# Kernel tuning notes

Measured on AMD Instinct MI355X. Metric: run time of the kernel, lower is better.

The kernel has to match this reference:

```python
import jax, jax.numpy as jnp
import numpy as np
from jax.ops import segment_sum, segment_max

N, E = 50000, 500000
D_IN, D_H, D_OUT = 128, 256, 40
BN_EPS = 1e-5


def setup_inputs() -> dict:
    key = jax.random.key(0)
    ks = jax.random.split(key, 16)
    g = lambda k, shape, fan: jax.random.normal(k, shape, jnp.float32) * (1.0 / np.sqrt(fan))
    inp = {
        "x": jax.random.normal(ks[0], (N, D_IN), jnp.float32),
        "edge_index": jax.random.randint(ks[1], (2, E), 0, N, jnp.int64),
        # GAT (heads=1)
        "W_gat": g(ks[2], (D_IN, D_H), D_IN),
        "att_src": g(ks[3], (D_H,), D_H),
        "att_dst": g(ks[4], (D_H,), D_H),
        "b_gat": jnp.zeros((D_H,), jnp.float32),
        # GIN MLP
        "W_gin1": g(ks[5], (D_IN, D_H), D_IN),
        "b_gin1": jnp.zeros((D_H,), jnp.float32),
        "W_gin2": g(ks[6], (D_H, D_H), D_H),
        "b_gin2": jnp.zeros((D_H,), jnp.float32),
        # GCN
        "W_gcn": g(ks[7], (D_IN, D_H), D_IN),
        "b_gcn": jnp.zeros((D_H,), jnp.float32),
        # BatchNorm1d(3*hidden)
        "gamma": jnp.ones((3 * D_H,), jnp.float32),
        "beta": jnp.zeros((3 * D_H,), jnp.float32),
        # head
        "W_lin": g(ks[8], (3 * D_H, D_H), 3 * D_H),
        "b_lin": jnp.zeros((D_H,), jnp.float32),
        "W_lin2": g(ks[9], (D_H, D_OUT), D_H),
        "b_lin2": jnp.zeros((D_OUT,), jnp.float32),
    }
    return inp


def _forward(x, edge_index, W_gat, att_src, att_dst, b_gat, W_gin1, b_gin1,
             W_gin2, b_gin2, W_gcn, b_gcn, gamma, beta, W_lin, b_lin, W_lin2, b_lin2):
    n = x.shape[0]
    src, dst = edge_index[0], edge_index[1]
    loop = jnp.arange(n, dtype=src.dtype)
    src_sl = jnp.concatenate([src, loop])  # edges + self-loops (GAT/GCN)
    dst_sl = jnp.concatenate([dst, loop])

    # ---- GATConv (1 head), messages src -> dst, softmax over dst ----
    xs = x @ W_gat                                   # [N, H]
    a = jax.nn.leaky_relu(xs @ att_src, negative_slope=0.2) if False else None
    e = (xs @ att_src)[src_sl] + (xs @ att_dst)[dst_sl]   # [E+N]
    e = jax.nn.leaky_relu(e, negative_slope=0.2)
    m = segment_max(e, dst_sl, num_segments=n)
    w = jnp.exp(e - m[dst_sl])
    denom = segment_sum(w, dst_sl, num_segments=n)
    alpha = w / denom[dst_sl]
    x_gat = segment_sum(alpha[:, None] * xs[src_sl], dst_sl, num_segments=n) + b_gat

    # ---- GINConv (eps=0): MLP(x + sum_neighbors x_j) ----
    agg = segment_sum(x[src], dst, num_segments=n)
    h = x + agg
    x_gin = jax.nn.relu(h @ W_gin1 + b_gin1) @ W_gin2 + b_gin2

    # ---- GCNConv: symmetric normalization with self-loops ----
    deg = segment_sum(jnp.ones_like(dst_sl, dtype=x.dtype), dst_sl, num_segments=n)
    dis = jax.lax.rsqrt(jnp.maximum(deg, 1.0))  # deg >= 1 due to self-loops
    norm = dis[src_sl] * dis[dst_sl]
    xw = x @ W_gcn
    x_gcn = segment_sum(norm[:, None] * xw[src_sl], dst_sl, num_segments=n) + b_gcn

    # ---- concat -> BN (training-mode batch stats) -> ReLU -> MLP head ----
    xc = jnp.concatenate([x_gat, x_gin, x_gcn], axis=1)  # [N, 3H]
    mu = jnp.mean(xc, axis=0)
    var = jnp.mean((xc - mu) ** 2, axis=0)
    xb = (xc - mu) * jax.lax.rsqrt(var + BN_EPS) * gamma + beta
    h2 = jax.nn.relu(jax.nn.relu(xb) @ W_lin + b_lin)
    return h2 @ W_lin2 + b_lin2


def reference(x, edge_index, W_gat, att_src, att_dst, b_gat, W_gin1, b_gin1,
              W_gin2, b_gin2, W_gcn, b_gcn, gamma, beta, W_lin, b_lin, W_lin2, b_lin2):
    return _forward(x, edge_index, W_gat, att_src, att_dst, b_gat, W_gin1, b_gin1,
                    W_gin2, b_gin2, W_gcn, b_gcn, gamma, beta, W_lin, b_lin, W_lin2, b_lin2)
```

## Files before the change

### kernel.cpp

```cpp
#include <hip/hip_runtime.h>
#include <math.h>

#define NN 50000
#define NE 500000

typedef __attribute__((ext_vector_type(8))) short short8;
typedef __attribute__((ext_vector_type(4))) float f32x4;

__device__ __forceinline__ float leaky02(float x) { return x > 0.f ? x : 0.2f * x; }
__device__ __forceinline__ ushort f2b(float f) {
    uint u = __float_as_uint(f);
    u += 0x7fffu + ((u >> 16) & 1u);
    return (ushort)(u >> 16);
}
__device__ __forceinline__ float b2f(ushort h) { return __uint_as_float(((uint)h) << 16); }
__device__ __forceinline__ float b2f_lo(uint w) { return __uint_as_float(w << 16); }
__device__ __forceinline__ float b2f_hi(uint w) { return __uint_as_float(w & 0xffff0000u); }
__device__ __forceinline__ uint pack2(float a, float b) {
    return (uint)f2b(a) | ((uint)f2b(b) << 16);
}

__global__ void mm_wt(const float* __restrict__ W, ushort* __restrict__ Wt, int K, int Nc)
{
    int idx = blockIdx.x * 256 + threadIdx.x;
    if (idx >= K * Nc) return;
    int n = idx / K, k = idx - n * K;
    Wt[idx] = f2b(W[(size_t)k * Nc + n]);
}

__global__ void mm_attvec(const float* __restrict__ W, const float* __restrict__ as_,
                          const float* __restrict__ ad_, float* __restrict__ va, float* __restrict__ vd)
{
    int i = threadIdx.x;
    const float* vec = (i < 128) ? as_ : ad_;
    int k = i & 127;
    float s = 0.f;
    for (int j = 0; j < 256; ++j) s += W[(size_t)k * 256 + j] * vec[j];
    if (i < 128) va[k] = s; else vd[k] = s;
}

__global__ __launch_bounds__(256) void mm_cvt_es(const float* __restrict__ x,
                                                 const float* __restrict__ va, const float* __restrict__ vd,
                                                 ushort* __restrict__ xb,
                                                 float* __restrict__ es, float* __restrict__ ed)
{
    int node = blockIdx.x * 4 + (threadIdx.x >> 6);
    int lane = threadIdx.x & 63;
    if (node >= NN) return;
    float2 xv = *(const float2*)(x + (size_t)node * 128 + lane * 2);
    float2 a = *(const float2*)(va + lane * 2);
    float2 b = *(const float2*)(vd + lane * 2);
    *(uint*)(xb + (size_t)node * 128 + lane * 2) = pack2(xv.x, xv.y);
    float s = xv.x * a.x + xv.y * a.y;
    float d = xv.x * b.x + xv.y * b.y;
    #pragma unroll
    for (int off = 32; off; off >>= 1) {
        s += __shfl_down(s, off);
        d += __shfl_down(d, off);
    }
    if (lane == 0) { es[node] = s; ed[node] = d; }
}

__global__ void mm_count(const int* __restrict__ dst, int* __restrict__ deg)
{
    int e = blockIdx.x * 256 + threadIdx.x;
    if (e >= NE) return;
    atomicAdd(&deg[dst[e]], 1);
}

__global__ __launch_bounds__(256) void mm_scan1(const int* __restrict__ deg, int* __restrict__ part)
{
    __shared__ int red[256];
    int i = blockIdx.x * 256 + threadIdx.x;
    red[threadIdx.x] = (i < NN) ? deg[i] : 0;
    __syncthreads();
    for (int off = 128; off; off >>= 1) {
        if (threadIdx.x < off) red[threadIdx.x] += red[threadIdx.x + off];
        __syncthreads();
    }
    if (threadIdx.x == 0) part[blockIdx.x] = red[0];
}

__global__ __launch_bounds__(256) void mm_scan2(int* __restrict__ part, int nb)
{
    __shared__ int tile[256];
    int t = threadIdx.x;
    int v = (t < nb) ? part[t] : 0;
    tile[t] = v; __syncthreads();
    for (int off = 1; off < 256; off <<= 1) {
        int a = (t >= off) ? tile[t - off] : 0;
        __syncthreads();
        tile[t] += a;
        __syncthreads();
    }
    if (t < nb) part[t] = tile[t] - v;
}

__global__ __launch_bounds__(256) void mm_scan3(const int* __restrict__ deg, const int* __restrict__ part,
                                                int* __restrict__ row_ptr, int* __restrict__ cursor)
{
    __shared__ int tile[256];
    int t = threadIdx.x;
    int i = blockIdx.x * 256 + t;
    int v = (i < NN) ? deg[i] : 0;
    tile[t] = v; __syncthreads();
    for (int off = 1; off < 256; off <<= 1) {
        int a = (t >= off) ? tile[t - off] : 0;
        __syncthreads();
        tile[t] += a;
        __syncthreads();
    }
    if (i < NN) {
        int ex = part[blockIdx.x] + tile[t] - v;
        row_ptr[i] = ex;
        cursor[i] = ex;
    }
    if (i == 0) row_ptr[NN] = NE;
}

__global__ void mm_fill(const int* __restrict__ src, const int* __restrict__ dst,
                        int* __restrict__ cursor, int* __restrict__ csr_src)
{
    int e = blockIdx.x * 256 + threadIdx.x;
    if (e >= NE) return;
    int pos = atomicAdd(&cursor[dst[e]], 1);
    csr_src[pos] = src[e];
}

__global__ void mm_dis(const int* __restrict__ row_ptr, float* __restrict__ dis)
{
    int i = blockIdx.x * 256 + threadIdx.x;
    if (i >= NN) return;
    dis[i] = rsqrtf((float)(row_ptr[i + 1] - row_ptr[i] + 1));
}

__global__ __launch_bounds__(256) void mm_node_agg(
    const int* __restrict__ row_ptr, const int* __restrict__ csr_src,
    const float* __restrict__ es, const float* __restrict__ ed,
    const float* __restrict__ dis,
    const ushort* __restrict__ xb, ushort* __restrict__ aggb)
{
    int d = blockIdx.x * 4 + (threadIdx.x >> 6);
    int lane = threadIdx.x & 63;
    if (d >= NN) return;
    int start = row_ptr[d], end = row_ptr[d + 1];
    float edd = ed[d], disd = dis[d];
    float selfv = leaky02(es[d] + edd);

    int myidx = -1; float myl = -3.0e38f, mynw = 0.f;
    if (start + lane < end) {
        myidx = csr_src[start + lane];
        myl = leaky02(es[myidx] + edd);
        mynw = dis[myidx] * disd;
    }
    float lmax = fmaxf(selfv, myl);
    for (int e = start + 64 + lane; e < end; e += 64)
        lmax = fmaxf(lmax, leaky02(es[csr_src[e]] + edd));
    #pragma unroll
    for (int off = 1; off < 64; off <<= 1) lmax = fmaxf(lmax, __shfl_xor(lmax, off));
    float m = lmax;

    float lsum = (myidx >= 0) ? __expf(myl - m) : 0.f;
    if (lane == 0) lsum += __expf(selfv - m);
    for (int e = start + 64 + lane; e < end; e += 64)
        lsum += __expf(leaky02(es[csr_src[e]] + edd) - m);
    #pragma unroll
    for (int off = 1; off < 64; off <<= 1) lsum += __shfl_xor(lsum, off);
    float inv = 1.f / lsum;
    float myal = __expf(myl - m) * inv;

    float aself = __expf(selfv - m) * inv;
    float d2 = disd * disd;
    uint wself = *(const uint*)(xb + (size_t)d * 128 + lane * 2);
    float x0 = b2f_lo(wself), x1 = b2f_hi(wself);
    float gat0 = aself * x0, gat1 = aself * x1;
    float gin0 = x0, gin1 = x1;
    float gcn0 = d2 * x0, gcn1 = d2 * x1;

    for (int base = start; base < end; base += 64) {
        int cnt = min(64, end - base);
        int bidx; float bal, bnw;
        if (base == start) { bidx = myidx; bal = myal; bnw = mynw; }
        else {
            bidx = -1; bal = 0.f; bnw = 0.f;
            if (base + lane < end) {
                bidx = csr_src[base + lane];
                bal = __expf(leaky02(es[bidx] + edd) - m) * inv;
                bnw = dis[bidx] * disd;
            }
        }
        int j = 0;
        for (; j + 4 <= cnt; j += 4) {
            int   s0 = __shfl(bidx, j),     s1 = __shfl(bidx, j + 1);
            int   s2 = __shfl(bidx, j + 2), s3 = __shfl(bidx, j + 3);
            float a0 = __shfl(bal, j),      a1 = __shfl(bal, j + 1);
            float a2 = __shfl(bal, j + 2),  a3 = __shfl(bal, j + 3);
            float n0 = __shfl(bnw, j),      n1 = __shfl(bnw, j + 1);
            float n2 = __shfl(bnw, j + 2),  n3 = __shfl(bnw, j + 3);
            uint w0 = *(const uint*)(xb + (size_t)s0 * 128 + lane * 2);
            uint w1 = *(const uint*)(xb + (size_t)s1 * 128 + lane * 2);
            uint w2 = *(const uint*)(xb + (size_t)s2 * 128 + lane * 2);
            uint w3 = *(const uint*)(xb + (size_t)s3 * 128 + lane * 2);
            float p0, p1;
            p0 = b2f_lo(w0); p1 = b2f_hi(w0);
            gat0 += a0 * p0; gat1 += a0 * p1; gin0 += p0; gin1 += p1; gcn0 += n0 * p0; gcn1 += n0 * p1;
            p0 = b2f_lo(w1); p1 = b2f_hi(w1);
            gat0 += a1 * p0; gat1 += a1 * p1; gin0 += p0; gin1 += p1; gcn0 += n1 * p0; gcn1 += n1 * p1;
            p0 = b2f_lo(w2); p1 = b2f_hi(w2);
            gat0 += a2 * p0; gat1 += a2 * p1; gin0 += p0; gin1 += p1; gcn0 += n2 * p0; gcn1 += n2 * p1;
            p0 = b2f_lo(w3); p1 = b2f_hi(w3);
            gat0 += a3 * p0; gat1 += a3 * p1; gin0 += p0; gin1 += p1; gcn0 += n3 * p0; gcn1 += n3 * p1;
        }
        for (; j < cnt; ++j) {
            int   s0 = __shfl(bidx, j);
            float a0 = __shfl(bal, j);
            float n0 = __shfl(bnw, j);
            uint w0 = *(const uint*)(xb + (size_t)s0 * 128 + lane * 2);
            float p0 = b2f_lo(w0), p1 = b2f_hi(w0);
            gat0 += a0 * p0; gat1 += a0 * p1; gin0 += p0; gin1 += p1; gcn0 += n0 * p0; gcn1 += n0 * p1;
        }
    }
    ushort* orow = aggb + (size_t)d * 384;
    *(uint*)(orow + lane * 2)       = pack2(gat0, gat1);
    *(uint*)(orow + 128 + lane * 2) = pack2(gin0, gin1);
    *(uint*)(orow + 256 + lane * 2) = pack2(gcn0, gcn1);
}

__device__ __forceinline__ void gemm_core(
    const ushort* __restrict__ A, int lda, const ushort* __restrict__ Bt,
    const float* __restrict__ bias, float* __restrict__ stats,
    ushort* __restrict__ Cb, int ldc, int M, int K, int relu,
    ushort* lds)
{
    const int tid = threadIdx.x;
    const int wave = tid >> 6, lane = tid & 63;
    const int row0 = blockIdx.x * 128;
    const int col0 = blockIdx.y * 128;

    int arow0 = min(row0 + wave * 16 + (lane >> 2), M - 1);
    int arow1 = min(row0 + 64 + wave * 16 + (lane >> 2), M - 1);
    int brow0 = col0 + wave * 16 + (lane >> 2);
    int brow1 = col0 + 64 + wave * 16 + (lane >> 2);
    const ushort* pa0 = A + (size_t)arow0 * lda + (lane & 3) * 8;
    const ushort* pa1 = A + (size_t)arow1 * lda + (lane & 3) * 8;
    const ushort* pb0 = Bt + (size_t)brow0 * K + (lane & 3) * 8;
    const ushort* pb1 = Bt + (size_t)brow1 * K + (lane & 3) * 8;
    const int wr = (wave >> 1) * 64, wc = (wave & 1) * 64;

    f32x4 zero = {0.f, 0.f, 0.f, 0.f};
    f32x4 acc[4][4];
    #pragma unroll
    for (int m = 0; m < 4; ++m)
        #pragma unroll
        for (int n = 0; n < 4; ++n) acc[m][n] = zero;

    const int nt = K >> 5;

#define STAGE_C(bufi) { \
    ushort* Lb = lds + (bufi) * 8192; \
    __builtin_amdgcn_global_load_lds((const __attribute__((address_space(1))) void*)pa0, \
        (__attribute__((address_space(3))) void*)(Lb + wave * 512), 16, 0, 0); \
    __builtin_amdgcn_global_load_lds((const __attribute__((address_space(1))) void*)pa1, \
        (__attribute__((address_space(3))) void*)(Lb + 2048 + wave * 512), 16, 0, 0); \
    __builtin_amdgcn_global_load_lds((const __attribute__((address_space(1))) void*)pb0, \
        (__attribute__((address_space(3))) void*)(Lb + 4096 + wave * 512), 16, 0, 0); \
    __builtin_amdgcn_global_load_lds((const __attribute__((address_space(1))) void*)pb1, \
        (__attribute__((address_space(3))) void*)(Lb + 6144 + wave * 512), 16, 0, 0); \
    pa0 += 32; pa1 += 32; pb0 += 32; pb1 += 32; }

    STAGE_C(0);
    for (int t = 0; t < nt; ++t) {
        int cur = t & 1;
        if (t + 1 < nt) {
            STAGE_C(cur ^ 1);
            asm volatile("s_waitcnt vmcnt(4) lgkmcnt(0)" ::: "memory");
        } else {
            asm volatile("s_waitcnt vmcnt(0) lgkmcnt(0)" ::: "memory");
        }
        __builtin_amdgcn_s_barrier();
        const ushort* As = lds + cur * 8192;
        const ushort* Bs = As + 4096;
        short8 a[4], b[4];
        #pragma unroll
        for (int m = 0; m < 4; ++m)
            a[m] = *(const short8*)&As[(wr + m * 16 + (lane & 15)) * 32 + (lane >> 4) * 8];
        #pragma unroll
        for (int n = 0; n < 4; ++n)
            b[n] = *(const short8*)&Bs[(wc + n * 16 + (lane & 15)) * 32 + (lane >> 4) * 8];
        #pragma unroll
        for (int m = 0; m < 4; ++m)
            #pragma unroll
            for (int n = 0; n < 4; ++n)
                acc[m][n] = __builtin_amdgcn_mfma_f32_16x16x32_bf16(a[m], b[n], acc[m][n], 0, 0, 0);
        if (t + 1 < nt) __builtin_amdgcn_s_barrier();
    }
#undef STAGE_C

    #pragma unroll
    for (int n = 0; n < 4; ++n) {
        int col = col0 + wc + n * 16 + (lane & 15);
        float bb = bias ? bias[col] : 0.f;
        float s_acc = 0.f, q_acc = 0.f;
        #pragma unroll
        for (int m = 0; m < 4; ++m) {
            int rb = row0 + wr + m * 16 + (lane >> 4) * 4;
            #pragma unroll
            for (int r = 0; r < 4; ++r) {
                int row = rb + r;
                if (row < M) {
                    float v = acc[m][n][r] + bb;
                    if (relu) v = fmaxf(v, 0.f);
                    Cb[(size_t)row * ldc + col] = f2b(v);
                    s_acc += v; q_acc += v * v;
                }
            }
        }
        if (stats) {
            s_acc += __shfl_xor(s_acc, 16); q_acc += __shfl_xor(q_acc, 16);
            s_acc += __shfl_xor(s_acc, 32); q_acc += __shfl_xor(q_acc, 32);
            if (lane < 16) {
                unsafeAtomicAdd(&stats[col], s_acc);
                unsafeAtomicAdd(&stats[768 + col], q_acc);
            }
        }
    }
}

__global__ __launch_bounds__(256) void mm_gemm3(
    const ushort* __restrict__ aggb,
    const ushort* __restrict__ wt_gat, const ushort* __restrict__ wt_gin1, const ushort* __restrict__ wt_gcn,
    const float* __restrict__ b_gat, const float* __restrict__ b_gin1, const float* __restrict__ b_gcn,
    float* __restrict__ bnsum,
    ushort* __restrict__ xcb, ushort* __restrict__ hid_b)
{
    __shared__ ushort lds[16384];
    const ushort* A; const ushort* Bt; const float* bias; float* stats; ushort* Cb; int ldc; int relu;
    if (blockIdx.z == 0)      { A = aggb;       Bt = wt_gat;  bias = b_gat;  stats = bnsum;       Cb = xcb;       ldc = 768; relu = 0; }
    else if (blockIdx.z == 1) { A = aggb + 128; Bt = wt_gin1; bias = b_gin1; stats = nullptr;     Cb = hid_b;     ldc = 256; relu = 1; }
    else                      { A = aggb + 256; Bt = wt_gcn;  bias = b_gcn;  stats = bnsum + 512; Cb = xcb + 512; ldc = 768; relu = 0; }
    gemm_core(A, 384, Bt, bias, stats, Cb, ldc, NN, 128, relu, lds);
}

__global__ __launch_bounds__(256) void mm_gemm_bf(
    const ushort* __restrict__ A, int lda, const ushort* __restrict__ Bt,
    const float* __restrict__ bias, float* __restrict__ stats,
    ushort* __restrict__ Cb, int ldc, int M, int K, int relu)
{
    __shared__ ushort lds[16384];
    gemm_core(A, lda, Bt, bias, stats, Cb, ldc, M, K, relu, lds);
}

__device__ __forceinline__ uint4 bn_relu_pack_l(uint4 w, const float* sc, const float* sh, int c)
{
    uint4 o;
    o.x = pack2(fmaxf(b2f_lo(w.x) * sc[c + 0] + sh[c + 0], 0.f), fmaxf(b2f_hi(w.x) * sc[c + 1] + sh[c + 1], 0.f));
    o.y = pack2(fmaxf(b2f_lo(w.y) * sc[c + 2] + sh[c + 2], 0.f), fmaxf(b2f_hi(w.y) * sc[c + 3] + sh[c + 3], 0.f));
    o.z = pack2(fmaxf(b2f_lo(w.z) * sc[c + 4] + sh[c + 4], 0.f), fmaxf(b2f_hi(w.z) * sc[c + 5] + sh[c + 5], 0.f));
    o.w = pack2(fmaxf(b2f_lo(w.w) * sc[c + 6] + sh[c + 6], 0.f), fmaxf(b2f_hi(w.w) * sc[c + 7] + sh[c + 7], 0.f));
    return o;
}

__global__ __launch_bounds__(256) void mm_gemm_bn(
    const ushort* __restrict__ A, const ushort* __restrict__ Bt,
    const float* __restrict__ bias,
    const float* __restrict__ sc, const float* __restrict__ sh,
    ushort* __restrict__ Cb, int ldc, int M)
{
    const int K = 768, lda = 768;
    __shared__ ushort lds[16384];
    __shared__ float sc_l[768], sh_l[768];
    const int tid = threadIdx.x;
    for (int i = tid; i < 768; i += 256) { sc_l[i] = sc[i]; sh_l[i] = sh[i]; }

    const int wave = tid >> 6, lane = tid & 63;
    const int row0 = blockIdx.x * 128;
    const int col0 = blockIdx.y * 128;

    int arow0 = min(row0 + wave * 16 + (lane >> 2), M - 1);
    int arow1 = min(row0 + 64 + wave * 16 + (lane >> 2), M - 1);
    int brow0 = col0 + wave * 16 + (lane >> 2);
    int brow1 = col0 + 64 + wave * 16 + (lane >> 2);
    const ushort* pa0 = A + (size_t)arow0 * lda + (lane & 3) * 8;
    const ushort* pa1 = A + (size_t)arow1 * lda + (lane & 3) * 8;
    const ushort* pb0 = Bt + (size_t)brow0 * K + (lane & 3) * 8;
    const ushort* pb1 = Bt + (size_t)brow1 * K + (lane & 3) * 8;
    const int wr = (wave >> 1) * 64, wc = (wave & 1) * 64;

    f32x4 zero = {0.f, 0.f, 0.f, 0.f};
    f32x4 acc[4][4];
    #pragma unroll
    for (int m = 0; m < 4; ++m)
        #pragma unroll
        for (int n = 0; n < 4; ++n) acc[m][n] = zero;

    const int nt = K >> 5;

#define STAGE_B(bufi) { \
    ushort* Lb = lds + (bufi) * 8192; \
    __builtin_amdgcn_global_load_lds((const __attribute__((address_space(1))) void*)pb0, \
        (__attribute__((address_space(3))) void*)(Lb + 4096 + wave * 512), 16, 0, 0); \
    __builtin_amdgcn_global_load_lds((const __attribute__((address_space(1))) void*)pb1, \
        (__attribute__((address_space(3))) void*)(Lb + 6144 + wave * 512), 16, 0, 0); \
    pb0 += 32; pb1 += 32; }

    uint4 w0 = *(const uint4*)pa0, w1 = *(const uint4*)pa1;
    pa0 += 32; pa1 += 32;
    STAGE_B(0);
    __syncthreads();
    {
        int c = (lane & 3) * 8;
        *(uint4*)(lds + wave * 512 + lane * 8) = bn_relu_pack_l(w0, sc_l, sh_l, c);
        *(uint4*)(lds + 2048 + wave * 512 + lane * 8) = bn_relu_pack_l(w1, sc_l, sh_l, c);
    }

    for (int t = 0; t < nt; ++t) {
        int cur = t & 1;
        bool more = (t + 1 < nt);
        uint4 w0n, w1n;
        if (more) {
            w0n = *(const uint4*)pa0; w1n = *(const uint4*)pa1;
            pa0 += 32; pa1 += 32;
            STAGE_B(cur ^ 1);
            asm volatile("s_waitcnt vmcnt(4) lgkmcnt(0)" ::: "memory");
        } else {
            asm volatile("s_waitcnt vmcnt(0) lgkmcnt(0)" ::: "memory");
        }
        __builtin_amdgcn_s_barrier();
        const ushort* As = lds + cur * 8192;
        const ushort* Bs = As + 4096;
        short8 a[4], b[4];
        #pragma unroll
        for (int m = 0; m < 4; ++m)
            a[m] = *(const short8*)&As[(wr + m * 16 + (lane & 15)) * 32 + (lane >> 4) * 8];
        #pragma unroll
        for (int n = 0; n < 4; ++n)
            b[n] = *(const short8*)&Bs[(wc + n * 16 + (lane & 15)) * 32 + (lane >> 4) * 8];
        #pragma unroll
        for (int m = 0; m < 4; ++m)
            #pragma unroll
            for (int n = 0; n < 4; ++n)
                acc[m][n] = __builtin_amdgcn_mfma_f32_16x16x32_bf16(a[m], b[n], acc[m][n], 0, 0, 0);
        if (more) {
            int c = (t + 1) * 32 + (lane & 3) * 8;
            ushort* Ln = lds + (cur ^ 1) * 8192;
            *(uint4*)(Ln + wave * 512 + lane * 8) = bn_relu_pack_l(w0n, sc_l, sh_l, c);
            *(uint4*)(Ln + 2048 + wave * 512 + lane * 8) = bn_relu_pack_l(w1n, sc_l, sh_l, c);
            __builtin_amdgcn_s_barrier();
        }
    }
#undef STAGE_B

    #pragma unroll
    for (int n = 0; n < 4; ++n) {
        int col = col0 + wc + n * 16 + (lane & 15);
        float bb = bias[col];
        #pragma unroll
        for (int m = 0; m < 4; ++m) {
            int rb = row0 + wr + m * 16 + (lane >> 4) * 4;
            #pragma unroll
            for (int r = 0; r < 4; ++r) {
                int row = rb + r;
                if (row < M)
                    Cb[(size_t)row * ldc + col] = f2b(fmaxf(acc[m][n][r] + bb, 0.f));
            }
        }
    }
}

__global__ void mm_bn_fin(const float* __restrict__ sums, const float* __restrict__ gamma,
                          const float* __restrict__ beta,
                          float* __restrict__ scale, float* __restrict__ shift)
{
    int c = blockIdx.x * 256 + threadIdx.x;
    if (c >= 768) return;
    float inv = 1.f / (float)NN;
    float mu = sums[c] * inv;
    float ex2 = sums[768 + c] * inv;
    float var = fmaxf(ex2 - mu * mu, 0.f);
    float rs = rsqrtf(var + 1e-5f);
    float sc = gamma[c] * rs;
    scale[c] = sc;
    shift[c] = beta[c] - mu * sc;
}

__global__ __launch_bounds__(256) void mm_head2(const ushort* __restrict__ h2b, const float* __restrict__ W2,
                                                const float* __restrict__ b2, float* __restrict__ out)
{
    __shared__ float Ws[256 * 40];
    for (int i = threadIdx.x; i < 256 * 40; i += 256) Ws[i] = W2[i];
    __syncthreads();
    int row = blockIdx.x * 32 + (threadIdx.x >> 3);
    int cg = (threadIdx.x & 7) * 5;
    if (row >= NN) return;
    const ushort* hr = h2b + (size_t)row * 256;
    float acc[5] = {0, 0, 0, 0, 0};
    for (int k = 0; k < 256; k += 8) {
        uint4 w = *(const uint4*)(hr + k);
        float a0 = b2f_lo(w.x), a1 = b2f_hi(w.x), a2 = b2f_lo(w.y), a3 = b2f_hi(w.y);
        float a4 = b2f_lo(w.z), a5 = b2f_hi(w.z), a6 = b2f_lo(w.w), a7 = b2f_hi(w.w);
        #pragma unroll
        for (int j = 0; j < 5; ++j) {
            acc[j] += a0 * Ws[(k + 0) * 40 + cg + j] + a1 * Ws[(k + 1) * 40 + cg + j]
                    + a2 * Ws[(k + 2) * 40 + cg + j] + a3 * Ws[(k + 3) * 40 + cg + j]
                    + a4 * Ws[(k + 4) * 40 + cg + j] + a5 * Ws[(k + 5) * 40 + cg + j]
                    + a6 * Ws[(k + 6) * 40 + cg + j] + a7 * Ws[(k + 7) * 40 + cg + j];
        }
    }
    #pragma unroll
    for (int j = 0; j < 5; ++j) out[(size_t)row * 40 + cg + j] = acc[j] + b2[cg + j];
}

extern "C" void kernel_launch(void* const* d_in, const int* in_sizes, int n_in,
                              void* d_out, int out_size, void* d_ws, size_t ws_size,
                              hipStream_t stream)
{
    const float* x      = (const float*)d_in[0];
    const int*   ei     = (const int*)d_in[1];
    const float* W_gat  = (const float*)d_in[2];
    const float* att_s  = (const float*)d_in[3];
    const float* att_d  = (const float*)d_in[4];
    const float* b_gat  = (const float*)d_in[5];
    const float* W_gin1 = (const float*)d_in[6];
    const float* b_gin1 = (const float*)d_in[7];
    const float* W_gin2 = (const float*)d_in[8];
    const float* b_gin2 = (const float*)d_in[9];
    const float* W_gcn  = (const float*)d_in[10];
    const float* b_gcn  = (const float*)d_in[11];
    const float* gamma  = (const float*)d_in[12];
    const float* beta   = (const float*)d_in[13];
    const float* W_lin  = (const float*)d_in[14];
    const float* b_lin  = (const float*)d_in[15];
    const float* W_lin2 = (const float*)d_in[16];
    const float* b_lin2 = (const float*)d_in[17];
    const int* src = ei;
    const int* dst = ei + NE;
    float* out = (float*)d_out;

    float* ws = (float*)d_ws;
    size_t off = 0;
    ushort* xb      = (ushort*)(ws + off); off += (size_t)NN * 64;
    ushort* aggb    = (ushort*)(ws + off); off += (size_t)NN * 192;
    ushort* hid_b   = (ushort*)(ws + off); off += (size_t)NN * 128;
    ushort* xcb     = (ushort*)(ws + off); off += (size_t)NN * 384;
    float* es       = ws + off; off += NN;
    float* ed       = ws + off; off += NN;
    float* dis      = ws + off; off += NN;
    float* va       = ws + off; off += 128;
    float* vd       = ws + off; off += 128;
    float* bnsum    = ws + off; off += 1536;
    float* bscale   = ws + off; off += 768;
    float* bshift   = ws + off; off += 768;
    ushort* wt_gat  = (ushort*)(ws + off); off += 128 * 256 / 2;
    ushort* wt_gin1 = (ushort*)(ws + off); off += 128 * 256 / 2;
    ushort* wt_gin2 = (ushort*)(ws + off); off += 256 * 256 / 2;
    ushort* wt_gcn  = (ushort*)(ws + off); off += 128 * 256 / 2;
    ushort* wt_lin  = (ushort*)(ws + off); off += 768 * 256 / 2;
    int* part       = (int*)(ws + off); off += 256;
    int* row_ptr    = (int*)(ws + off); off += NN + 1;
    int* cursor     = (int*)(ws + off); off += NN;
    int* csr_src    = (int*)(ws + off); off += NE;

    dim3 blk(256);
    dim3 gemm_grid((NN + 127) / 128, 2);
    dim3 gemm_grid3((NN + 127) / 128, 2, 3);
    const int NB = (NN + 255) / 256;

    hipMemsetAsync(bnsum, 0, 1536 * sizeof(float), stream);
    hipMemsetAsync(cursor, 0, NN * sizeof(int), stream);

    mm_wt<<<(128 * 256 + 255) / 256, blk, 0, stream>>>(W_gat, wt_gat, 128, 256);
    mm_wt<<<(128 * 256 + 255) / 256, blk, 0, stream>>>(W_gin1, wt_gin1, 128, 256);
    mm_wt<<<(256 * 256 + 255) / 256, blk, 0, stream>>>(W_gin2, wt_gin2, 256, 256);
    mm_wt<<<(128 * 256 + 255) / 256, blk, 0, stream>>>(W_gcn, wt_gcn, 128, 256);
    mm_wt<<<(768 * 256 + 255) / 256, blk, 0, stream>>>(W_lin, wt_lin, 768, 256);
    mm_attvec<<<1, blk, 0, stream>>>(W_gat, att_s, att_d, va, vd);

    mm_cvt_es<<<(NN + 3) / 4, blk, 0, stream>>>(x, va, vd, xb, es, ed);

    mm_count<<<(NE + 255) / 256, blk, 0, stream>>>(dst, cursor);
    mm_scan1<<<NB, blk, 0, stream>>>(cursor, part);
    mm_scan2<<<1, blk, 0, stream>>>(part, NB);
    mm_scan3<<<NB, blk, 0, stream>>>(cursor, part, row_ptr, cursor);
    mm_dis<<<(NN + 255) / 256, blk, 0, stream>>>(row_ptr, dis);
    mm_fill<<<(NE + 255) / 256, blk, 0, stream>>>(src, dst, cursor, csr_src);

    mm_node_agg<<<(NN + 3) / 4, blk, 0, stream>>>(row_ptr, csr_src, es, ed, dis, xb, aggb);

    mm_gemm3<<<gemm_grid3, blk, 0, stream>>>(aggb, wt_gat, wt_gin1, wt_gcn,
                                             b_gat, b_gin1, b_gcn, bnsum, xcb, hid_b);
    mm_gemm_bf<<<gemm_grid, blk, 0, stream>>>(hid_b, 256, wt_gin2, b_gin2, bnsum + 256,
                                              xcb + 256, 768, NN, 256, 0);

    mm_bn_fin<<<3, blk, 0, stream>>>(bnsum, gamma, beta, bscale, bshift);

    mm_gemm_bn<<<gemm_grid, blk, 0, stream>>>(xcb, wt_lin, b_lin, bscale, bshift, hid_b, 256, NN);
    mm_head2<<<(NN + 31) / 32, blk, 0, stream>>>(hid_b, W_lin2, b_lin2, out);
}
```

Measured before the change: 377.1 us.

## Merge weight transposes, sort CSR segments, use per-block BN partial sums

Combines five weight transpose/convert launches into one kernel. Adds a warp bitonic sort of each destination's source list after CSR fill, making edge order deterministic and possibly improving gather locality. Replaces global atomics for BatchNorm statistics with per-row-block partial slots that the finalize kernel reduces, removing atomic contention at the cost of a larger memset and a serial reduction loop.

```diff
diff --git a/kernel.cpp b/kernel.cpp
--- a/kernel.cpp
+++ b/kernel.cpp
@@ -3,6 +3,7 @@
 
 #define NN 50000
 #define NE 500000
+#define NRB 391
 
 typedef __attribute__((ext_vector_type(8))) short short8;
 typedef __attribute__((ext_vector_type(4))) float f32x4;
@@ -20,12 +21,24 @@
     return (uint)f2b(a) | ((uint)f2b(b) << 16);
 }
 
-__global__ void mm_wt(const float* __restrict__ W, ushort* __restrict__ Wt, int K, int Nc)
+__global__ void mm_wt_all(const float* __restrict__ Wg, const float* __restrict__ Wi1,
+                          const float* __restrict__ Wi2, const float* __restrict__ Wc,
+                          const float* __restrict__ Wl,
+                          ushort* __restrict__ tg, ushort* __restrict__ ti1,
+                          ushort* __restrict__ ti2, ushort* __restrict__ tc,
+                          ushort* __restrict__ tl)
 {
     int idx = blockIdx.x * 256 + threadIdx.x;
-    if (idx >= K * Nc) return;
-    int n = idx / K, k = idx - n * K;
-    Wt[idx] = f2b(W[(size_t)k * Nc + n]);
+    const float* W; ushort* T; int K; int base;
+    if (idx < 32768)       { W = Wg;  T = tg;  K = 128; base = 0; }
+    else if (idx < 65536)  { W = Wi1; T = ti1; K = 128; base = 32768; }
+    else if (idx < 131072) { W = Wi2; T = ti2; K = 256; base = 65536; }
+    else if (idx < 163840) { W = Wc;  T = tc;  K = 128; base = 131072; }
+    else if (idx < 360448) { W = Wl;  T = tl;  K = 768; base = 163840; }
+    else return;
+    int i = idx - base;
+    int n = i / K, k = i - n * K;
+    T[i] = f2b(W[(size_t)k * 256 + n]);
 }
 
 __global__ void mm_attvec(const float* __restrict__ W, const float* __restrict__ as_,
@@ -125,6 +138,28 @@
     if (e >= NE) return;
     int pos = atomicAdd(&cursor[dst[e]], 1);
     csr_src[pos] = src[e];
+}
+
+__global__ __launch_bounds__(256) void mm_sortseg(const int* __restrict__ row_ptr, int* __restrict__ csr_src)
+{
+    int d = blockIdx.x * 4 + (threadIdx.x >> 6);
+    int lane = threadIdx.x & 63;
+    if (d >= NN) return;
+    int start = row_ptr[d], end = row_ptr[d + 1];
+    int deg = end - start;
+    if (deg <= 1 || deg > 64) return;
+    int v = (start + lane < end) ? csr_src[start + lane] : 0x7fffffff;
+    #pragma unroll
+    for (int k = 2; k <= 64; k <<= 1) {
+        #pragma unroll
+        for (int j = k >> 1; j > 0; j >>= 1) {
+            int o = __shfl_xor(v, j);
+            bool asc = ((lane & k) == 0);
+            bool low = ((lane & j) == 0);
+            v = (asc == low) ? min(v, o) : max(v, o);
+        }
+    }
+    if (start + lane < end) csr_src[start + lane] = v;
 }
 
 __global__ void mm_dis(const int* __restrict__ row_ptr, float* __restrict__ dis)
@@ -228,7 +263,7 @@
 
 __device__ __forceinline__ void gemm_core(
     const ushort* __restrict__ A, int lda, const ushort* __restrict__ Bt,
-    const float* __restrict__ bias, float* __restrict__ stats,
+    const float* __restrict__ bias, float* __restrict__ pstat, int colbase,
     ushort* __restrict__ Cb, int ldc, int M, int K, int relu,
     ushort* lds)
 {
@@ -315,12 +350,13 @@
                 }
             }
         }
-        if (stats) {
+        if (pstat) {
             s_acc += __shfl_xor(s_acc, 16); q_acc += __shfl_xor(q_acc, 16);
             s_acc += __shfl_xor(s_acc, 32); q_acc += __shfl_xor(q_acc, 32);
             if (lane < 16) {
-                unsafeAtomicAdd(&stats[col], s_acc);
-                unsafeAtomicAdd(&stats[768 + col], q_acc);
+                size_t slot = (size_t)(colbase + col) * NRB + blockIdx.x;
+                unsafeAtomicAdd(&pstat[slot], s_acc);
+                unsafeAtomicAdd(&pstat[(size_t)768 * NRB + slot], q_acc);
             }
         }
     }
@@ -330,24 +366,25 @@
     const ushort* __restrict__ aggb,
     const ushort* __restrict__ wt_gat, const ushort* __restrict__ wt_gin1, const ushort* __restrict__ wt_gcn,
     const float* __restrict__ b_gat, const float* __restrict__ b_gin1, const float* __restrict__ b_gcn,
-    float* __restrict__ bnsum,
+    float* __restrict__ pstat,
     ushort* __restrict__ xcb, ushort* __restrict__ hid_b)
 {
     __shared__ ushort lds[16384];
-    const ushort* A; const ushort* Bt; const float* bias; float* stats; ushort* Cb; int ldc; int relu;
-    if (blockIdx.z == 0)      { A = aggb;       Bt = wt_gat;  bias = b_gat;  stats = bnsum;       Cb = xcb;       ldc = 768; relu = 0; }
-    else if (blockIdx.z == 1) { A = aggb + 128; Bt = wt_gin1; bias = b_gin1; stats = nullptr;     Cb = hid_b;     ldc = 256; relu = 1; }
-    else                      { A = aggb + 256; Bt = wt_gcn;  bias = b_gcn;  stats = bnsum + 512; Cb = xcb + 512; ldc = 768; relu = 0; }
-    gemm_core(A, 384, Bt, bias, stats, Cb, ldc, NN, 128, relu, lds);
+    if (blockIdx.z == 0)
+        gemm_core(aggb,       384, wt_gat,  b_gat,  pstat,   0,   xcb,       768, NN, 128, 0, lds);
+    else if (blockIdx.z == 1)
+        gemm_core(aggb + 128, 384, wt_gin1, b_gin1, nullptr, 0,   hid_b,     256, NN, 128, 1, lds);
+    else
+        gemm_core(aggb + 256, 384, wt_gcn,  b_gcn,  pstat,   512, xcb + 512, 768, NN, 128, 0, lds);
 }
 
 __global__ __launch_bounds__(256) void mm_gemm_bf(
     const ushort* __restrict__ A, int lda, const ushort* __restrict__ Bt,
-    const float* __restrict__ bias, float* __restrict__ stats,
+    const float* __restrict__ bias, float* __restrict__ pstat, int colbase,
     ushort* __restrict__ Cb, int ldc, int M, int K, int relu)
 {
     __shared__ ushort lds[16384];
-    gemm_core(A, lda, Bt, bias, stats, Cb, ldc, M, K, relu, lds);
+    gemm_core(A, lda, Bt, bias, pstat, colbase, Cb, ldc, M, K, relu, lds);
 }
 
 __device__ __forceinline__ uint4 bn_relu_pack_l(uint4 w, const float* sc, const float* sh, int c)
@@ -467,15 +504,19 @@
     }
 }
 
-__global__ void mm_bn_fin(const float* __restrict__ sums, const float* __restrict__ gamma,
+__global__ void mm_bn_fin(const float* __restrict__ pstat, const float* __restrict__ gamma,
                           const float* __restrict__ beta,
                           float* __restrict__ scale, float* __restrict__ shift)
 {
     int c = blockIdx.x * 256 + threadIdx.x;
     if (c >= 768) return;
-    float inv = 1.f / (float)NN;
-    float mu = sums[c] * inv;
-    float ex2 = sums[768 + c] * inv;
+    const float* ps = pstat + (size_t)c * NRB;
+    const float* pq = pstat + (size_t)768 * NRB + (size_t)c * NRB;
+    float s = 0.f, q = 0.f;
+    for (int rb = 0; rb < NRB; ++rb) { s += ps[rb]; q += pq[rb]; }
+    float invn = 1.f / (float)NN;
+    float mu = s * invn;
+    float ex2 = q * invn;
     float var = fmaxf(ex2 - mu * mu, 0.f);
     float rs = rsqrtf(var + 1e-5f);
     float sc = gamma[c] * rs;
@@ -547,7 +588,7 @@
     float* dis      = ws + off; off += NN;
     float* va       = ws + off; off += 128;
     float* vd       = ws + off; off += 128;
-    float* bnsum    = ws + off; off += 1536;
+    float* pstat    = ws + off; off += (size_t)1536 * NRB;
     float* bscale   = ws + off; off += 768;
     float* bshift   = ws + off; off += 768;
     ushort* wt_gat  = (ushort*)(ws + off); off += 128 * 256 / 2;
@@ -561,18 +602,15 @@
     int* csr_src    = (int*)(ws + off); off += NE;
 
     dim3 blk(256);
-    dim3 gemm_grid((NN + 127) / 128, 2);
-    dim3 gemm_grid3((NN + 127) / 128, 2, 3);
+    dim3 gemm_grid(NRB, 2);
+    dim3 gemm_grid3(NRB, 2, 3);
     const int NB = (NN + 255) / 256;
 
-    hipMemsetAsync(bnsum, 0, 1536 * sizeof(float), stream);
+    hipMemsetAsync(pstat, 0, (size_t)1536 * NRB * sizeof(float), stream);
     hipMemsetAsync(cursor, 0, NN * sizeof(int), stream);
 
-    mm_wt<<<(128 * 256 + 255) / 256, blk, 0, stream>>>(W_gat, wt_gat, 128, 256);
-    mm_wt<<<(128 * 256 + 255) / 256, blk, 0, stream>>>(W_gin1, wt_gin1, 128, 256);
-    mm_wt<<<(256 * 256 + 255) / 256, blk, 0, stream>>>(W_gin2, wt_gin2, 256, 256);
-    mm_wt<<<(128 * 256 + 255) / 256, blk, 0, stream>>>(W_gcn, wt_gcn, 128, 256);
-    mm_wt<<<(768 * 256 + 255) / 256, blk, 0, stream>>>(W_lin, wt_lin, 768, 256);
+    mm_wt_all<<<(360448 + 255) / 256, blk, 0, stream>>>(W_gat, W_gin1, W_gin2, W_gcn, W_lin,
+                                                        wt_gat, wt_gin1, wt_gin2, wt_gcn, wt_lin);
     mm_attvec<<<1, blk, 0, stream>>>(W_gat, att_s, att_d, va, vd);
 
     mm_cvt_es<<<(NN + 3) / 4, blk, 0, stream>>>(x, va, vd, xb, es, ed);
@@ -583,15 +621,16 @@
     mm_scan3<<<NB, blk, 0, stream>>>(cursor, part, row_ptr, cursor);
     mm_dis<<<(NN + 255) / 256, blk, 0, stream>>>(row_ptr, dis);
     mm_fill<<<(NE + 255) / 256, blk, 0, stream>>>(src, dst, cursor, csr_src);
+    mm_sortseg<<<(NN + 3) / 4, blk, 0, stream>>>(row_ptr, csr_src);
 
     mm_node_agg<<<(NN + 3) / 4, blk, 0, stream>>>(row_ptr, csr_src, es, ed, dis, xb, aggb);
 
     mm_gemm3<<<gemm_grid3, blk, 0, stream>>>(aggb, wt_gat, wt_gin1, wt_gcn,
-                                             b_gat, b_gin1, b_gcn, bnsum, xcb, hid_b);
-    mm_gemm_bf<<<gemm_grid, blk, 0, stream>>>(hid_b, 256, wt_gin2, b_gin2, bnsum + 256,
+                                             b_gat, b_gin1, b_gcn, pstat, xcb, hid_b);
+    mm_gemm_bf<<<gemm_grid, blk, 0, stream>>>(hid_b, 256, wt_gin2, b_gin2, pstat, 256,
                                               xcb + 256, 768, NN, 256, 0);
 
-    mm_bn_fin<<<3, blk, 0, stream>>>(bnsum, gamma, beta, bscale, bshift);
+    mm_bn_fin<<<3, blk, 0, stream>>>(pstat, gamma, beta, bscale, bshift);
 
     mm_gemm_bn<<<gemm_grid, blk, 0, stream>>>(xcb, wt_lin, b_lin, bscale, bshift, hid_b, 256, NN);
     mm_head2<<<(NN + 31) / 32, blk, 0, stream>>>(hid_b, W_lin2, b_lin2, out);
```

New measurement: 418.9 us. 1.11x slower.
